# Kernel optimization log

Measured on AMD Instinct MI355X. Metric: run time of the kernel, lower is better.

## Reference

```python
import jax, jax.numpy as jnp
import numpy as np

B, S, H = 2, 1024, 2048
D = 256          # index_dimension = min(index.embedding_dimension, hidden_size)
R = 32           # LoRA rank
K = 4            # index_k neighbors per query token
N_DB = 100000    # rows in the external index


def setup_inputs() -> dict:
    key = jax.random.key(0)
    ks = jax.random.split(key, 7)
    return {
        "hidden_states": jax.random.normal(ks[0], (B, S, H), jnp.float32),
        "db_keys": jax.random.normal(ks[1], (N_DB, D), jnp.float32),
        "db_values": jax.random.normal(ks[2], (N_DB, D), jnp.float32),
        "wq_in": jax.random.normal(ks[3], (H, R), jnp.float32) * 0.02,
        "wq_out": jax.random.normal(ks[4], (R, D), jnp.float32) * 0.02,
        "wv_in": jax.random.normal(ks[5], (D, R), jnp.float32) * 0.02,
        "wv_out": jax.random.normal(ks[6], (R, H), jnp.float32) * 0.02,
    }


def reference(hidden_states, db_keys, db_values, wq_in, wq_out, wv_in, wv_out):
    b, s, h = hidden_states.shape
    d = wq_out.shape[1]
    # query LoRA projection: hidden -> r -> index_dim
    q = (hidden_states @ wq_in) @ wq_out            # [B, S, D]

    # external k-NN lookup (exact L2 top-k over index table), no_grad in torch
    qf = q.reshape(b * s, d)                        # [B*S, D]
    qn = jnp.sum(qf * qf, axis=-1, keepdims=True)   # [B*S, 1]
    kn = jnp.sum(db_keys * db_keys, axis=-1)        # [N_DB]
    dist = qn - 2.0 * (qf @ db_keys.T) + kn[None, :]  # [B*S, N_DB]
    _, idx = jax.lax.top_k(-dist, K)                # [B*S, K] nearest neighbors

    # gather KV and reshape to [B, S*K, D] (matches torch view calls)
    kv_key = jax.lax.stop_gradient(db_keys[idx]).reshape(b, s * K, d)
    kv_val = jax.lax.stop_gradient(db_values[idx]).reshape(b, s * K, d)

    # SDPA, is_causal=True with Lq != Lk: top-left aligned tril mask (j <= i)
    scale = 1.0 / np.sqrt(d).astype(np.float32)
    scores = jnp.einsum('bqd,bkd->bqk', q, kv_key) * scale  # [B, S, S*K]
    mask = jnp.arange(s * K)[None, :] <= jnp.arange(s)[:, None]
    scores = jnp.where(mask[None, :, :], scores, jnp.finfo(scores.dtype).min)
    attn = jax.nn.softmax(scores, axis=-1)
    out = jnp.einsum('bqk,bkd->bqd', attn, kv_val)  # [B, S, D]

    # value LoRA projection: index_dim -> r -> hidden
    return (out @ wv_in) @ wv_out                   # [B, S, H]
```

## Files before the change

### kernel.cpp

```cpp
#include <hip/hip_runtime.h>
#include <cfloat>

#define B_   2
#define S_   1024
#define H_   2048
#define D_   256
#define R_   32
#define K_   4
#define NDB_ 100000

#define TSEL 256
#define NSEL (B_ * TSEL)

#define NCHUNK     61
#define CHUNK_ROWS 1664
#define TILES      13
#define NT         128
#define MT         64
#define KC         64
#define LSTR       68

#define NEG_INF  (-3.0e38f)
#define IDX_MAX  0x7fffffff

#define OFF_Q     0
#define OFF_KN    0x200000
#define OFF_PS    0x280000
#define OFF_PI    0x300000
#define OFF_IDX   0x380000
#define OFF_CAND  0x3A0000
#define OFF_KVT   0x400000
#define OFF_AO    0x600000
#define OFF_KVV   0x800000
#define OFF_DBK16 0xA00000

typedef unsigned short ushort_t;
typedef unsigned int   uint_t;
typedef __attribute__((ext_vector_type(8)))  __bf16 bf16x8;
typedef __attribute__((ext_vector_type(16))) float  f32x16;

__device__ __forceinline__ void ins4(float sc, int n, float s[4], int id[4]) {
  if (sc > s[3] || (sc == s[3] && n < id[3])) {
    s[3] = sc; id[3] = n;
#pragma unroll
    for (int k = 3; k > 0; --k) {
      if (s[k] > s[k - 1] || (s[k] == s[k - 1] && id[k] < id[k - 1])) {
        float ts = s[k]; s[k] = s[k - 1]; s[k - 1] = ts;
        int ti = id[k]; id[k] = id[k - 1]; id[k - 1] = ti;
      }
    }
  }
}

__device__ __forceinline__ uint_t bfpack(float a, float b) {
  uint_t ua = __float_as_uint(a), ub = __float_as_uint(b);
  ua = (ua + 0x7fffu + ((ua >> 16) & 1u)) >> 16;
  ub = (ub + 0x7fffu + ((ub >> 16) & 1u)) >> 16;
  return ua | (ub << 16);
}

__global__ __launch_bounds__(256) void k_compute_q(
    const float* __restrict__ hidden, const float* __restrict__ wq_in,
    const float* __restrict__ wq_out, float* __restrict__ q) {
  __shared__ float hrow[H_];
  __shared__ float part[8][R_];
  __shared__ float q1[R_];
  const int m = blockIdx.x;
  const int t = threadIdx.x;
  const float* hp = hidden + (size_t)m * H_;
  ((float4*)hrow)[t]       = ((const float4*)hp)[t];
  ((float4*)hrow)[t + 256] = ((const float4*)hp)[t + 256];
  __syncthreads();
  const int r = t & 31, c = t >> 5;
  float p = 0.f;
#pragma unroll 4
  for (int e = c * 256; e < c * 256 + 256; ++e)
    p = fmaf(hrow[e], wq_in[(size_t)e * R_ + r], p);
  part[c][r] = p;
  __syncthreads();
  if (t < R_) {
    float s = 0.f;
#pragma unroll
    for (int cc = 0; cc < 8; ++cc) s += part[cc][t];
    q1[t] = s;
  }
  __syncthreads();
  float acc = 0.f;
#pragma unroll
  for (int rr = 0; rr < R_; ++rr) acc = fmaf(q1[rr], wq_out[rr * D_ + t], acc);
  q[(size_t)m * D_ + t] = acc;
}

__global__ __launch_bounds__(256) void k_kn_cvt(const float* __restrict__ dbk,
                                               float* __restrict__ kn,
                                               ushort_t* __restrict__ dbk16) {
  const int w = threadIdx.x >> 6, l = threadIdx.x & 63;
  const int n = blockIdx.x * 4 + w;
  if (n >= NDB_) return;
  const float4 v = ((const float4*)(dbk + (size_t)n * D_))[l];
  uint2 p; p.x = bfpack(v.x, v.y); p.y = bfpack(v.z, v.w);
  ((uint2*)(dbk16 + (size_t)n * D_))[l] = p;
  float s = v.x * v.x + v.y * v.y + v.z * v.z + v.w * v.w;
#pragma unroll
  for (int off = 32; off; off >>= 1) s += __shfl_down(s, off);
  if (l == 0) kn[n] = s;
}

__global__ __launch_bounds__(256) void k_kn(const float* __restrict__ dbk,
                                            float* __restrict__ kn) {
  const int w = threadIdx.x >> 6, l = threadIdx.x & 63;
  const int n = blockIdx.x * 4 + w;
  if (n >= NDB_) return;
  const float4 v = ((const float4*)(dbk + (size_t)n * D_))[l];
  float s = v.x * v.x + v.y * v.y + v.z * v.z + v.w * v.w;
#pragma unroll
  for (int off = 32; off; off >>= 1) s += __shfl_down(s, off);
  if (l == 0) kn[n] = s;
}

__global__ __launch_bounds__(256, 2) void k_knn_mfma(
    const float* __restrict__ q, const ushort_t* __restrict__ dbk16,
    const float* __restrict__ kn, float* __restrict__ pscore,
    int* __restrict__ pidx) {
  __shared__ __align__(16) char smem[65536];
  ushort_t* sA = (ushort_t*)smem;
  ushort_t* sB = (ushort_t*)(smem + 32768);
  float*    sS = (float*)(smem + 32768);

  const int tid = threadIdx.x;
  const int wv = tid >> 6, ln = tid & 63;
  const int lm = ln & 31, lh = ln >> 5;
  const int tx = tid & 15, ty = tid >> 4;
  const int qb = blockIdx.x, chunk = blockIdx.y;
  const int row_base = chunk * CHUNK_ROWS;

  {
    const int m = tid & 63, cg = tid >> 6;
    const int sq = qb * MT + m;
    const float* qp = q + ((size_t)((sq >> 8) * S_ + (sq & 255))) * D_;
#pragma unroll
    for (int cc = 0; cc < 8; ++cc) {
      const int c = cg * 8 + cc;
      const float4 v0 = *(const float4*)(qp + c * 8);
      const float4 v1 = *(const float4*)(qp + c * 8 + 4);
      uint4 pk;
      pk.x = bfpack(v0.x, v0.y); pk.y = bfpack(v0.z, v0.w);
      pk.z = bfpack(v1.x, v1.y); pk.w = bfpack(v1.z, v1.w);
      *(uint4*)&sA[(m * 32 + (c ^ (m & 7))) * 8] = pk;
    }
  }

  float s4[4][4]; int i4[4][4];
#pragma unroll
  for (int a = 0; a < 4; ++a)
#pragma unroll
    for (int b = 0; b < 4; ++b) { s4[a][b] = NEG_INF; i4[a][b] = IDX_MAX; }

  for (int tile = 0; tile < TILES; ++tile) {
    const int row0 = row_base + tile * NT;
    if (row0 >= NDB_) break;

    f32x16 acc0, acc1;
#pragma unroll
    for (int r = 0; r < 16; ++r) { acc0[r] = 0.f; acc1[r] = 0.f; }

    for (int kh = 0; kh < 2; ++kh) {
      __syncthreads();
      {
        const int n_in = ln >> 4;
        const int p    = ln & 15;
#pragma unroll
        for (int i = 0; i < 8; ++i) {
          const int nloc = wv * 32 + i * 4 + n_in;
          int krow = row0 + nloc; if (krow >= NDB_) krow = NDB_ - 1;
          const int c = p ^ (nloc & 7);
          const ushort_t* gp = dbk16 + (size_t)krow * D_ + (kh * 16 + c) * 8;
          ushort_t* lp = sB + (size_t)(wv * 32 + i * 4) * 128;
          __builtin_amdgcn_global_load_lds(
              (const __attribute__((address_space(1))) void*)gp,
              (__attribute__((address_space(3))) void*)lp, 16, 0, 0);
        }
      }
      __syncthreads();
      const int nB = wv * 32 + lm;
      const int bswz = nB & 7;
#pragma unroll
      for (int ks = 0; ks < 8; ++ks) {
        const int cA = kh * 16 + ks * 2 + lh;
        const bf16x8 a0 = *(const bf16x8*)&sA[(lm * 32 + (cA ^ (lm & 7))) * 8];
        const bf16x8 a1 = *(const bf16x8*)&sA[((32 + lm) * 32 + (cA ^ (lm & 7))) * 8];
        const bf16x8 bb = *(const bf16x8*)&sB[(nB * 16 + ((ks * 2 + lh) ^ bswz)) * 8];
        acc0 = __builtin_amdgcn_mfma_f32_32x32x16_bf16(a0, bb, acc0, 0, 0, 0);
        acc1 = __builtin_amdgcn_mfma_f32_32x32x16_bf16(a1, bb, acc1, 0, 0, 0);
      }
    }
    __syncthreads();

    {
      const int n = (tid >> 6) * 32 + lm;
#pragma unroll
      for (int r = 0; r < 16; ++r) {
        const int mrow = (r & 3) + 8 * (r >> 2) + 4 * lh;
        sS[mrow * 128 + n]        = acc0[r];
        sS[(32 + mrow) * 128 + n] = acc1[r];
      }
    }
    __syncthreads();

    {
      const int nbase = row0 + tx * 8;
      float knv[8]; int nok[8];
#pragma unroll
      for (int j = 0; j < 8; ++j) {
        nok[j] = (nbase + j < NDB_);
        knv[j] = nok[j] ? kn[nbase + j] : 0.f;
      }
#pragma unroll
      for (int qi = 0; qi < 4; ++qi) {
        const int m = ty * 4 + qi;
        const float4 v0 = *(const float4*)&sS[m * 128 + tx * 8];
        const float4 v1 = *(const float4*)&sS[m * 128 + tx * 8 + 4];
        const float sv[8] = {v0.x, v0.y, v0.z, v0.w, v1.x, v1.y, v1.z, v1.w};
        float v[8];
#pragma unroll
        for (int j = 0; j < 8; ++j)
          v[j] = nok[j] ? fmaf(2.f, sv[j], -knv[j]) : NEG_INF;
        const float mx = fmaxf(fmaxf(fmaxf(v[0], v[1]), fmaxf(v[2], v[3])),
                               fmaxf(fmaxf(v[4], v[5]), fmaxf(v[6], v[7])));
        if (mx >= s4[qi][3]) {
#pragma unroll
          for (int j = 0; j < 8; ++j)
            if (nok[j]) ins4(v[j], nbase + j, s4[qi], i4[qi]);
        }
      }
    }
  }

  __syncthreads();
  float* cs = (float*)smem;
  int*   ci = (int*)(smem + 64 * 65 * 4);
#pragma unroll
  for (int qi = 0; qi < 4; ++qi)
#pragma unroll
    for (int k = 0; k < 4; ++k) {
      cs[(ty * 4 + qi) * 65 + tx * 4 + k] = s4[qi][k];
      ci[(ty * 4 + qi) * 65 + tx * 4 + k] = i4[qi][k];
    }
  __syncthreads();
  if (tid < 64) {
    float fs[4]; int fi[4];
#pragma unroll
    for (int k = 0; k < 4; ++k) { fs[k] = NEG_INF; fi[k] = IDX_MAX; }
    for (int c = 0; c < 64; ++c)
      ins4(cs[tid * 65 + c], ci[tid * 65 + c], fs, fi);
    const int sq = qb * MT + tid;
    float* po = pscore + ((size_t)sq * NCHUNK + chunk) * 4;
    int*   io = pidx   + ((size_t)sq * NCHUNK + chunk) * 4;
#pragma unroll
    for (int k = 0; k < 4; ++k) { po[k] = fs[k]; io[k] = fi[k]; }
  }
}

__global__ __launch_bounds__(256) void k_knn_partial(
    const float* __restrict__ q, const float* __restrict__ dbk,
    const float* __restrict__ kn, float* __restrict__ pscore,
    int* __restrict__ pidx) {
  __shared__ float smem[3 * KC * LSTR];
  float* sA  = smem;
  float* sB0 = smem + KC * LSTR;
  float* sB1 = smem + 2 * KC * LSTR;
  const int tid = threadIdx.x;
  const int tx = tid & 15, ty = tid >> 4;
  const int chunk = blockIdx.x, qb = blockIdx.y;
  const int arq = tid >> 2;
  const int aqd = (tid & 3) * 4;
  const int brk = tid >> 1;
  const int bh  = tid & 1;
  const int bcol = ((brk >> 3) << 2) | (brk & 3);
  float* sBw = (brk & 4) ? sB1 : sB0;
  const int sq_a = qb * MT + arq;
  const float* qsrc = q + ((size_t)((sq_a >> 8) * S_ + (sq_a & 255))) * D_;
  float s4[4][4]; int i4[4][4];
#pragma unroll
  for (int a = 0; a < 4; ++a)
#pragma unroll
    for (int b = 0; b < 4; ++b) { s4[a][b] = NEG_INF; i4[a][b] = IDX_MAX; }
  const int row_base = chunk * CHUNK_ROWS;
  for (int tile = 0; tile < TILES; ++tile) {
    const int row0 = row_base + tile * NT;
    if (row0 >= NDB_) break;
    int krow = row0 + brk; if (krow >= NDB_) krow = NDB_ - 1;
    const float* ksrc = dbk + (size_t)krow * D_;
    float acc[4][8];
#pragma unroll
    for (int a = 0; a < 4; ++a)
#pragma unroll
      for (int b = 0; b < 8; ++b) acc[a][b] = 0.f;
    for (int kc = 0; kc < 4; ++kc) {
      __syncthreads();
#pragma unroll
      for (int p = 0; p < 4; ++p) {
        const int kkl = p * 16 + aqd;
        const float4 v = *(const float4*)(qsrc + kc * KC + kkl);
        sA[(kkl + 0) * LSTR + arq] = v.x;
        sA[(kkl + 1) * LSTR + arq] = v.y;
        sA[(kkl + 2) * LSTR + arq] = v.z;
        sA[(kkl + 3) * LSTR + arq] = v.w;
      }
#pragma unroll
      for (int p = 0; p < 8; ++p) {
        const int kkl = bh * 32 + p * 4;
        const float4 v = *(const float4*)(ksrc + kc * KC + kkl);
        sBw[(kkl + 0) * LSTR + bcol] = v.x;
        sBw[(kkl + 1) * LSTR + bcol] = v.y;
        sBw[(kkl + 2) * LSTR + bcol] = v.z;
        sBw[(kkl + 3) * LSTR + bcol] = v.w;
      }
      __syncthreads();
#pragma unroll 4
      for (int kk = 0; kk < KC; ++kk) {
        const float4 a  = *(const float4*)&sA [kk * LSTR + ty * 4];
        const float4 b0 = *(const float4*)&sB0[kk * LSTR + tx * 4];
        const float4 b1 = *(const float4*)&sB1[kk * LSTR + tx * 4];
        const float av[4] = {a.x, a.y, a.z, a.w};
        const float bv[8] = {b0.x, b0.y, b0.z, b0.w, b1.x, b1.y, b1.z, b1.w};
#pragma unroll
        for (int qi = 0; qi < 4; ++qi)
#pragma unroll
          for (int nj = 0; nj < 8; ++nj)
            acc[qi][nj] = fmaf(av[qi], bv[nj], acc[qi][nj]);
      }
    }
#pragma unroll
    for (int nj = 0; nj < 8; ++nj) {
      const int n = row0 + tx * 8 + nj;
      if (n < NDB_) {
        const float knj = kn[n];
        ins4(2.f * acc[0][nj] - knj, n, s4[0], i4[0]);
        ins4(2.f * acc[1][nj] - knj, n, s4[1], i4[1]);
        ins4(2.f * acc[2][nj] - knj, n, s4[2], i4[2]);
        ins4(2.f * acc[3][nj] - knj, n, s4[3], i4[3]);
      }
    }
  }
  __syncthreads();
  float* cs = smem;
  int*   ci = (int*)(smem + 64 * 65);
#pragma unroll
  for (int qi = 0; qi < 4; ++qi)
#pragma unroll
    for (int k = 0; k < 4; ++k) {
      cs[(ty * 4 + qi) * 65 + tx * 4 + k] = s4[qi][k];
      ci[(ty * 4 + qi) * 65 + tx * 4 + k] = i4[qi][k];
    }
  __syncthreads();
  if (tid < 64) {
    float fs[4]; int fi[4];
#pragma unroll
    for (int k = 0; k < 4; ++k) { fs[k] = NEG_INF; fi[k] = IDX_MAX; }
    for (int c = 0; c < 64; ++c)
      ins4(cs[tid * 65 + c], ci[tid * 65 + c], fs, fi);
    const int sq = qb * MT + tid;
    float* po = pscore + ((size_t)sq * NCHUNK + chunk) * 4;
    int*   io = pidx   + ((size_t)sq * NCHUNK + chunk) * 4;
#pragma unroll
    for (int k = 0; k < 4; ++k) { po[k] = fs[k]; io[k] = fi[k]; }
  }
}

template <int RANKS>
__device__ __forceinline__ void merge_top(const float* __restrict__ pscore,
                                          const int* __restrict__ pidx,
                                          int* __restrict__ outp) {
  const int sq = blockIdx.x, l = threadIdx.x;
  float s4[4]; int i4[4];
#pragma unroll
  for (int k = 0; k < 4; ++k) { s4[k] = NEG_INF; i4[k] = IDX_MAX; }
  for (int c = l; c < NCHUNK * 4; c += 64)
    ins4(pscore[(size_t)sq * NCHUNK * 4 + c], pidx[(size_t)sq * NCHUNK * 4 + c], s4, i4);
#pragma unroll
  for (int r = 0; r < RANKS; ++r) {
    float s = s4[0]; int i = i4[0];
#pragma unroll
    for (int off = 32; off; off >>= 1) {
      float so = __shfl_down(s, off); int io = __shfl_down(i, off);
      if (so > s || (so == s && io < i)) { s = so; i = io; }
    }
    const float sw = __shfl(s, 0); const int iw = __shfl(i, 0);
    if (l == 0) outp[sq * RANKS + r] = iw;
    if (s4[0] == sw && i4[0] == iw) {
      s4[0] = s4[1]; i4[0] = i4[1];
      s4[1] = s4[2]; i4[1] = i4[2];
      s4[2] = s4[3]; i4[2] = i4[3];
      s4[3] = NEG_INF; i4[3] = IDX_MAX;
    }
  }
}

__global__ __launch_bounds__(64) void k_knn_merge4(const float* __restrict__ ps,
                                                   const int* __restrict__ pi,
                                                   int* __restrict__ knn_idx) {
  merge_top<4>(ps, pi, knn_idx);
}
__global__ __launch_bounds__(64) void k_knn_merge16(const float* __restrict__ ps,
                                                    const int* __restrict__ pi,
                                                    int* __restrict__ cand) {
  merge_top<16>(ps, pi, cand);
}

__global__ __launch_bounds__(256) void k_rescore(const float* __restrict__ q,
                                                 const float* __restrict__ dbk,
                                                 const float* __restrict__ kn,
                                                 const int* __restrict__ cand,
                                                 int* __restrict__ knn_idx) {
  __shared__ float scs[16];
  __shared__ int   sci[16];
  const int sq = blockIdx.x, wv = threadIdx.x >> 6, l = threadIdx.x & 63;
  const float* qp = q + ((size_t)((sq >> 8) * S_ + (sq & 255))) * D_;
  const float4 qv = ((const float4*)qp)[l];
  for (int cc = wv; cc < 16; cc += 4) {
    const int n = cand[sq * 16 + cc];
    const float4 kv = ((const float4*)(dbk + (size_t)n * D_))[l];
    float s = qv.x * kv.x + qv.y * kv.y + qv.z * kv.z + qv.w * kv.w;
#pragma unroll
    for (int off = 32; off; off >>= 1) s += __shfl_down(s, off);
    if (l == 0) { scs[cc] = 2.f * s - kn[n]; sci[cc] = n; }
  }
  __syncthreads();
  if (threadIdx.x == 0) {
    float s4[4]; int i4[4];
#pragma unroll
    for (int k = 0; k < 4; ++k) { s4[k] = NEG_INF; i4[k] = IDX_MAX; }
#pragma unroll
    for (int c = 0; c < 16; ++c) ins4(scs[c], sci[c], s4, i4);
#pragma unroll
    for (int k = 0; k < 4; ++k) knn_idx[sq * 4 + k] = i4[k];
  }
}

__global__ __launch_bounds__(256) void k_gather(const float* __restrict__ dbk,
                                                const float* __restrict__ dbv,
                                                const int* __restrict__ knn_idx,
                                                float* __restrict__ kvT,
                                                float* __restrict__ kvV) {
  const int b = blockIdx.x >> 6, j0 = (blockIdx.x & 63) * 16;
  const int w = threadIdx.x >> 6, l = threadIdx.x & 63;
  float* dstT = kvT + (size_t)b * D_ * 1024;
  float* dstV = kvV + (size_t)b * 1024 * D_;
  for (int jj = w; jj < 16; jj += 4) {
    const int j = j0 + jj;
    const int row = knn_idx[b * 1024 + j];
    const float4 kv = ((const float4*)(dbk + (size_t)row * D_))[l];
    dstT[(4 * l + 0) * 1024 + j] = kv.x;
    dstT[(4 * l + 1) * 1024 + j] = kv.y;
    dstT[(4 * l + 2) * 1024 + j] = kv.z;
    dstT[(4 * l + 3) * 1024 + j] = kv.w;
    const float4 vv = ((const float4*)(dbv + (size_t)row * D_))[l];
    ((float4*)(dstV + (size_t)j * D_))[l] = vv;
  }
}

__global__ __launch_bounds__(256) void k_attn(const float* __restrict__ qarr,
                                              const float* __restrict__ kvT,
                                              const float* __restrict__ kvV,
                                              float* __restrict__ attout) {
  __shared__ float qrow[D_];
  __shared__ float attw[1024];
  __shared__ float red1[4], red2[4];
  const int b = blockIdx.x >> 10, i = blockIdx.x & 1023;
  const int t = threadIdx.x;
  const int nk = i + 1;
  qrow[t] = qarr[((size_t)b * S_ + i) * D_ + t];
  __syncthreads();
  const int cmax = (nk + 255) >> 8;
  const float scale = 0.0625f;
  float sc[4]; float mloc = NEG_INF;
#pragma unroll
  for (int c = 0; c < 4; ++c) {
    sc[c] = NEG_INF;
    if (c < cmax) {
      const int j = c * 256 + t;
      float a = 0.f;
      const float* kp = kvT + (size_t)b * D_ * 1024 + j;
#pragma unroll 8
      for (int d = 0; d < D_; ++d) a = fmaf(qrow[d], kp[(size_t)d * 1024], a);
      if (j < nk) sc[c] = a * scale;
    }
    mloc = fmaxf(mloc, sc[c]);
  }
#pragma unroll
  for (int off = 32; off; off >>= 1) mloc = fmaxf(mloc, __shfl_down(mloc, off));
  if ((t & 63) == 0) red1[t >> 6] = mloc;
  __syncthreads();
  const float mmax = fmaxf(fmaxf(red1[0], red1[1]), fmaxf(red1[2], red1[3]));
  float sloc = 0.f; float pv[4];
#pragma unroll
  for (int c = 0; c < 4; ++c) {
    pv[c] = (sc[c] > NEG_INF * 0.5f) ? __expf(sc[c] - mmax) : 0.f;
    sloc += pv[c];
  }
#pragma unroll
  for (int off = 32; off; off >>= 1) sloc += __shfl_down(sloc, off);
  if ((t & 63) == 0) red2[t >> 6] = sloc;
  __syncthreads();
  const float inv = 1.f / (red2[0] + red2[1] + red2[2] + red2[3]);
#pragma unroll
  for (int c = 0; c < 4; ++c)
    if (c < cmax) attw[c * 256 + t] = pv[c] * inv;
  __syncthreads();
  const float* vb = kvV + (size_t)b * 1024 * D_;
  float a0 = 0.f, a1 = 0.f, a2 = 0.f, a3 = 0.f;
  int j = 0;
  for (; j + 4 <= nk; j += 4) {
    a0 = fmaf(attw[j + 0], vb[(size_t)(j + 0) * D_ + t], a0);
    a1 = fmaf(attw[j + 1], vb[(size_t)(j + 1) * D_ + t], a1);
    a2 = fmaf(attw[j + 2], vb[(size_t)(j + 2) * D_ + t], a2);
    a3 = fmaf(attw[j + 3], vb[(size_t)(j + 3) * D_ + t], a3);
  }
  for (; j < nk; ++j) a0 = fmaf(attw[j], vb[(size_t)j * D_ + t], a0);
  attout[((size_t)b * S_ + i) * D_ + t] = (a0 + a1) + (a2 + a3);
}

__global__ __launch_bounds__(256) void k_out(const float* __restrict__ attout,
                                             const float* __restrict__ wv_in,
                                             const float* __restrict__ wv_out,
                                             float* __restrict__ y) {
  __shared__ float row[D_];
  __shared__ float part[8][R_];
  __shared__ float t32[R_];
  const int m = blockIdx.x, t = threadIdx.x;
  row[t] = attout[(size_t)m * D_ + t];
  __syncthreads();
  const int r = t & 31, c = t >> 5;
  float p = 0.f;
#pragma unroll
  for (int d = c * 32; d < c * 32 + 32; ++d)
    p = fmaf(row[d], wv_in[d * R_ + r], p);
  part[c][r] = p;
  __syncthreads();
  if (t < R_) {
    float s = 0.f;
#pragma unroll
    for (int cc = 0; cc < 8; ++cc) s += part[cc][t];
    t32[t] = s;
  }
  __syncthreads();
  for (int hh = t; hh < H_; hh += 256) {
    float a = 0.f;
#pragma unroll
    for (int rr = 0; rr < R_; ++rr) a = fmaf(t32[rr], wv_out[rr * H_ + hh], a);
    y[(size_t)m * H_ + hh] = a;
  }
}

extern "C" void kernel_launch(void* const* d_in, const int* in_sizes, int n_in,
                              void* d_out, int out_size, void* d_ws, size_t ws_size,
                              hipStream_t stream) {
  const float* hidden  = (const float*)d_in[0];
  const float* db_keys = (const float*)d_in[1];
  const float* db_vals = (const float*)d_in[2];
  const float* wq_in   = (const float*)d_in[3];
  const float* wq_out  = (const float*)d_in[4];
  const float* wv_in   = (const float*)d_in[5];
  const float* wv_out  = (const float*)d_in[6];
  float* out = (float*)d_out;

  char* ws = (char*)d_ws;
  float*    q      = (float*)(ws + OFF_Q);
  float*    kn     = (float*)(ws + OFF_KN);
  float*    ps     = (float*)(ws + OFF_PS);
  int*      pi     = (int*)  (ws + OFF_PI);
  int*      idx    = (int*)  (ws + OFF_IDX);
  int*      cand   = (int*)  (ws + OFF_CAND);
  float*    kvT    = (float*)(ws + OFF_KVT);
  float*    attout = (float*)(ws + OFF_AO);
  float*    kvV    = (float*)(ws + OFF_KVV);
  ushort_t* dbk16  = (ushort_t*)(ws + OFF_DBK16);

  const size_t need = (size_t)OFF_DBK16 + (size_t)NDB_ * D_ * 2;

  k_compute_q<<<B_ * S_, 256, 0, stream>>>(hidden, wq_in, wq_out, q);
  if (ws_size >= need) {
    k_kn_cvt<<<(NDB_ + 3) / 4, 256, 0, stream>>>(db_keys, kn, dbk16);
    k_knn_mfma<<<dim3(8, NCHUNK), 256, 0, stream>>>(q, dbk16, kn, ps, pi);
    k_knn_merge16<<<NSEL, 64, 0, stream>>>(ps, pi, cand);
    k_rescore<<<NSEL, 256, 0, stream>>>(q, db_keys, kn, cand, idx);
  } else {
    k_kn<<<(NDB_ + 3) / 4, 256, 0, stream>>>(db_keys, kn);
    k_knn_partial<<<dim3(NCHUNK, 8), 256, 0, stream>>>(q, db_keys, kn, ps, pi);
    k_knn_merge4<<<NSEL, 64, 0, stream>>>(ps, pi, idx);
  }
  k_gather<<<2 * 64, 256, 0, stream>>>(db_keys, db_vals, idx, kvT, kvV);
  k_attn<<<B_ * S_, 256, 0, stream>>>(q, kvT, kvV, attout);
  k_out<<<B_ * S_, 256, 0, stream>>>(attout, wv_in, wv_out, out);
}
```

Measured before the change: 544.4 us.

## Restructure kNN MFMA kernel to hold DB keys in registers and score in-register

The MFMA kNN kernel now loads each wave's 32 database rows directly from global memory into registers as the A operand and keeps 128 query rows in LDS as the B operand. This removes the per-tile LDS staging of DB keys, the score round-trip through shared memory and most barriers, and top-4 selection now runs directly on the accumulator registers. The kn buffer is padded with large sentinel values so out-of-range rows drop out without bounds checks. The chunk count and tile sizes change (131 chunks of 768 rows), and partial-result buffers are aliased onto the later KV workspace. The trade-off is much higher register pressure (16 bf16x8 fragments plus four accumulators) and more partial results to merge.

```diff
diff --git a/kernel.cpp b/kernel.cpp
--- a/kernel.cpp
+++ b/kernel.cpp
@@ -8,14 +8,19 @@
 #define R_   32
 #define K_   4
 #define NDB_ 100000
+#define KN_PAD 2048
 
 #define TSEL 256
 #define NSEL (B_ * TSEL)
 
-#define NCHUNK     61
-#define CHUNK_ROWS 1664
-#define TILES      13
-#define NT         128
+#define NCHUNK     131
+#define CHUNK_ROWS 768
+#define TILES      6
+#define MTQ        128
+
+#define FB_NCHUNK     61
+#define FB_CHUNK_ROWS 1664
+#define FB_TILES      13
 #define MT         64
 #define KC         64
 #define LSTR       68
@@ -25,14 +30,12 @@
 
 #define OFF_Q     0
 #define OFF_KN    0x200000
-#define OFF_PS    0x280000
-#define OFF_PI    0x300000
-#define OFF_IDX   0x380000
-#define OFF_CAND  0x3A0000
-#define OFF_KVT   0x400000
-#define OFF_AO    0x600000
-#define OFF_KVV   0x800000
-#define OFF_DBK16 0xA00000
+#define OFF_IDX   0x280000
+#define OFF_CAND  0x290000
+#define OFF_KVT   0x300000
+#define OFF_AO    0x500000
+#define OFF_KVV   0x700000
+#define OFF_DBK16 0x900000
 
 typedef unsigned short ushort_t;
 typedef unsigned int   uint_t;
@@ -96,7 +99,8 @@
                                                ushort_t* __restrict__ dbk16) {
   const int w = threadIdx.x >> 6, l = threadIdx.x & 63;
   const int n = blockIdx.x * 4 + w;
-  if (n >= NDB_) return;
+  if (n >= NDB_ + KN_PAD) return;
+  if (n >= NDB_) { if (l == 0) kn[n] = 1.0e30f; return; }
   const float4 v = ((const float4*)(dbk + (size_t)n * D_))[l];
   uint2 p; p.x = bfpack(v.x, v.y); p.y = bfpack(v.z, v.w);
   ((uint2*)(dbk16 + (size_t)n * D_))[l] = p;
@@ -122,138 +126,112 @@
     const float* __restrict__ q, const ushort_t* __restrict__ dbk16,
     const float* __restrict__ kn, float* __restrict__ pscore,
     int* __restrict__ pidx) {
-  __shared__ __align__(16) char smem[65536];
-  ushort_t* sA = (ushort_t*)smem;
-  ushort_t* sB = (ushort_t*)(smem + 32768);
-  float*    sS = (float*)(smem + 32768);
+  __shared__ __align__(16) ushort_t sA16[MTQ * 256];
 
   const int tid = threadIdx.x;
-  const int wv = tid >> 6, ln = tid & 63;
+  const int w = tid >> 6, ln = tid & 63;
   const int lm = ln & 31, lh = ln >> 5;
-  const int tx = tid & 15, ty = tid >> 4;
   const int qb = blockIdx.x, chunk = blockIdx.y;
   const int row_base = chunk * CHUNK_ROWS;
 
   {
-    const int m = tid & 63, cg = tid >> 6;
-    const int sq = qb * MT + m;
+    const int m = tid >> 1, h = tid & 1;
+    const int sq = qb * MTQ + m;
     const float* qp = q + ((size_t)((sq >> 8) * S_ + (sq & 255))) * D_;
 #pragma unroll
-    for (int cc = 0; cc < 8; ++cc) {
-      const int c = cg * 8 + cc;
+    for (int ci = 0; ci < 16; ++ci) {
+      const int c = h * 16 + ci;
       const float4 v0 = *(const float4*)(qp + c * 8);
       const float4 v1 = *(const float4*)(qp + c * 8 + 4);
       uint4 pk;
       pk.x = bfpack(v0.x, v0.y); pk.y = bfpack(v0.z, v0.w);
       pk.z = bfpack(v1.x, v1.y); pk.w = bfpack(v1.z, v1.w);
-      *(uint4*)&sA[(m * 32 + (c ^ (m & 7))) * 8] = pk;
-    }
-  }
+      *(uint4*)&sA16[(m * 32 + (c ^ (m & 7))) * 8] = pk;
+    }
+  }
+  __syncthreads();
 
   float s4[4][4]; int i4[4][4];
 #pragma unroll
-  for (int a = 0; a < 4; ++a)
-#pragma unroll
-    for (int b = 0; b < 4; ++b) { s4[a][b] = NEG_INF; i4[a][b] = IDX_MAX; }
+  for (int g = 0; g < 4; ++g)
+#pragma unroll
+    for (int k = 0; k < 4; ++k) { s4[g][k] = NEG_INF; i4[g][k] = IDX_MAX; }
+
+  const int aswz = lm & 7;
 
   for (int tile = 0; tile < TILES; ++tile) {
-    const int row0 = row_base + tile * NT;
-    if (row0 >= NDB_) break;
-
-    f32x16 acc0, acc1;
-#pragma unroll
-    for (int r = 0; r < 16; ++r) { acc0[r] = 0.f; acc1[r] = 0.f; }
-
-    for (int kh = 0; kh < 2; ++kh) {
-      __syncthreads();
-      {
-        const int n_in = ln >> 4;
-        const int p    = ln & 15;
-#pragma unroll
-        for (int i = 0; i < 8; ++i) {
-          const int nloc = wv * 32 + i * 4 + n_in;
-          int krow = row0 + nloc; if (krow >= NDB_) krow = NDB_ - 1;
-          const int c = p ^ (nloc & 7);
-          const ushort_t* gp = dbk16 + (size_t)krow * D_ + (kh * 16 + c) * 8;
-          ushort_t* lp = sB + (size_t)(wv * 32 + i * 4) * 128;
-          __builtin_amdgcn_global_load_lds(
-              (const __attribute__((address_space(1))) void*)gp,
-              (__attribute__((address_space(3))) void*)lp, 16, 0, 0);
+    const int row0 = row_base + tile * 128;
+    int rowA = row0 + w * 32 + lm; if (rowA >= NDB_) rowA = NDB_ - 1;
+    const ushort_t* ap = dbk16 + (size_t)rowA * D_ + lh * 8;
+
+    bf16x8 aF[16];
+#pragma unroll
+    for (int ks = 0; ks < 16; ++ks)
+      aF[ks] = *(const bf16x8*)(ap + ks * 16);
+
+    const int knb = row0 + w * 32 + lh * 4;
+    const float4 kf0 = *(const float4*)&kn[knb];
+    const float4 kf1 = *(const float4*)&kn[knb + 8];
+    const float4 kf2 = *(const float4*)&kn[knb + 16];
+    const float4 kf3 = *(const float4*)&kn[knb + 24];
+    const float karr[16] = {kf0.x, kf0.y, kf0.z, kf0.w, kf1.x, kf1.y, kf1.z, kf1.w,
+                            kf2.x, kf2.y, kf2.z, kf2.w, kf3.x, kf3.y, kf3.z, kf3.w};
+
+    f32x16 acc[4];
+#pragma unroll
+    for (int g = 0; g < 4; ++g)
+#pragma unroll
+      for (int r = 0; r < 16; ++r) acc[g][r] = 0.f;
+
+#pragma unroll
+    for (int ks = 0; ks < 16; ++ks) {
+      const int pos = ((ks * 2 + lh) ^ aswz) * 8;
+#pragma unroll
+      for (int g = 0; g < 4; ++g) {
+        const bf16x8 bq = *(const bf16x8*)&sA16[(g * 32 + lm) * 256 + pos];
+        acc[g] = __builtin_amdgcn_mfma_f32_32x32x16_bf16(aF[ks], bq, acc[g], 0, 0, 0);
+      }
+    }
+
+#pragma unroll
+    for (int g = 0; g < 4; ++g) {
+      float v[16];
+#pragma unroll
+      for (int r = 0; r < 16; ++r) v[r] = fmaf(2.f, acc[g][r], -karr[r]);
+      float mx = v[0];
+#pragma unroll
+      for (int r = 1; r < 16; ++r) mx = fmaxf(mx, v[r]);
+      if (mx >= s4[g][3]) {
+#pragma unroll
+        for (int r = 0; r < 16; ++r) {
+          const int n = row0 + w * 32 + (r >> 2) * 8 + 4 * lh + (r & 3);
+          ins4(v[r], n, s4[g], i4[g]);
         }
       }
-      __syncthreads();
-      const int nB = wv * 32 + lm;
-      const int bswz = nB & 7;
-#pragma unroll
-      for (int ks = 0; ks < 8; ++ks) {
-        const int cA = kh * 16 + ks * 2 + lh;
-        const bf16x8 a0 = *(const bf16x8*)&sA[(lm * 32 + (cA ^ (lm & 7))) * 8];
-        const bf16x8 a1 = *(const bf16x8*)&sA[((32 + lm) * 32 + (cA ^ (lm & 7))) * 8];
-        const bf16x8 bb = *(const bf16x8*)&sB[(nB * 16 + ((ks * 2 + lh) ^ bswz)) * 8];
-        acc0 = __builtin_amdgcn_mfma_f32_32x32x16_bf16(a0, bb, acc0, 0, 0, 0);
-        acc1 = __builtin_amdgcn_mfma_f32_32x32x16_bf16(a1, bb, acc1, 0, 0, 0);
-      }
-    }
-    __syncthreads();
-
-    {
-      const int n = (tid >> 6) * 32 + lm;
-#pragma unroll
-      for (int r = 0; r < 16; ++r) {
-        const int mrow = (r & 3) + 8 * (r >> 2) + 4 * lh;
-        sS[mrow * 128 + n]        = acc0[r];
-        sS[(32 + mrow) * 128 + n] = acc1[r];
-      }
-    }
-    __syncthreads();
-
-    {
-      const int nbase = row0 + tx * 8;
-      float knv[8]; int nok[8];
-#pragma unroll
-      for (int j = 0; j < 8; ++j) {
-        nok[j] = (nbase + j < NDB_);
-        knv[j] = nok[j] ? kn[nbase + j] : 0.f;
-      }
-#pragma unroll
-      for (int qi = 0; qi < 4; ++qi) {
-        const int m = ty * 4 + qi;
-        const float4 v0 = *(const float4*)&sS[m * 128 + tx * 8];
-        const float4 v1 = *(const float4*)&sS[m * 128 + tx * 8 + 4];
-        const float sv[8] = {v0.x, v0.y, v0.z, v0.w, v1.x, v1.y, v1.z, v1.w};
-        float v[8];
-#pragma unroll
-        for (int j = 0; j < 8; ++j)
-          v[j] = nok[j] ? fmaf(2.f, sv[j], -knv[j]) : NEG_INF;
-        const float mx = fmaxf(fmaxf(fmaxf(v[0], v[1]), fmaxf(v[2], v[3])),
-                               fmaxf(fmaxf(v[4], v[5]), fmaxf(v[6], v[7])));
-        if (mx >= s4[qi][3]) {
-#pragma unroll
-          for (int j = 0; j < 8; ++j)
-            if (nok[j]) ins4(v[j], nbase + j, s4[qi], i4[qi]);
-        }
-      }
-    }
-  }
-
-  __syncthreads();
-  float* cs = (float*)smem;
-  int*   ci = (int*)(smem + 64 * 65 * 4);
-#pragma unroll
-  for (int qi = 0; qi < 4; ++qi)
+    }
+  }
+
+  __syncthreads();
+  float* cs = (float*)sA16;
+  int*   ci = (int*)((char*)sA16 + 128 * 33 * 4 + 64);
+#pragma unroll
+  for (int g = 0; g < 4; ++g) {
+    const int qrow = g * 32 + lm;
+    const int src = w * 8 + lh * 4;
 #pragma unroll
     for (int k = 0; k < 4; ++k) {
-      cs[(ty * 4 + qi) * 65 + tx * 4 + k] = s4[qi][k];
-      ci[(ty * 4 + qi) * 65 + tx * 4 + k] = i4[qi][k];
-    }
-  __syncthreads();
-  if (tid < 64) {
+      cs[qrow * 33 + src + k] = s4[g][k];
+      ci[qrow * 33 + src + k] = i4[g][k];
+    }
+  }
+  __syncthreads();
+  if (tid < MTQ) {
     float fs[4]; int fi[4];
 #pragma unroll
     for (int k = 0; k < 4; ++k) { fs[k] = NEG_INF; fi[k] = IDX_MAX; }
-    for (int c = 0; c < 64; ++c)
-      ins4(cs[tid * 65 + c], ci[tid * 65 + c], fs, fi);
-    const int sq = qb * MT + tid;
+    for (int c = 0; c < 32; ++c)
+      ins4(cs[tid * 33 + c], ci[tid * 33 + c], fs, fi);
+    const int sq = qb * MTQ + tid;
     float* po = pscore + ((size_t)sq * NCHUNK + chunk) * 4;
     int*   io = pidx   + ((size_t)sq * NCHUNK + chunk) * 4;
 #pragma unroll
@@ -285,9 +263,9 @@
   for (int a = 0; a < 4; ++a)
 #pragma unroll
     for (int b = 0; b < 4; ++b) { s4[a][b] = NEG_INF; i4[a][b] = IDX_MAX; }
-  const int row_base = chunk * CHUNK_ROWS;
-  for (int tile = 0; tile < TILES; ++tile) {
-    const int row0 = row_base + tile * NT;
+  const int row_base = chunk * FB_CHUNK_ROWS;
+  for (int tile = 0; tile < FB_TILES; ++tile) {
+    const int row0 = row_base + tile * 128;
     if (row0 >= NDB_) break;
     int krow = row0 + brk; if (krow >= NDB_) krow = NDB_ - 1;
     const float* ksrc = dbk + (size_t)krow * D_;
@@ -361,8 +339,8 @@
     for (int c = 0; c < 64; ++c)
       ins4(cs[tid * 65 + c], ci[tid * 65 + c], fs, fi);
     const int sq = qb * MT + tid;
-    float* po = pscore + ((size_t)sq * NCHUNK + chunk) * 4;
-    int*   io = pidx   + ((size_t)sq * NCHUNK + chunk) * 4;
+    float* po = pscore + ((size_t)sq * FB_NCHUNK + chunk) * 4;
+    int*   io = pidx   + ((size_t)sq * FB_NCHUNK + chunk) * 4;
 #pragma unroll
     for (int k = 0; k < 4; ++k) { po[k] = fs[k]; io[k] = fi[k]; }
   }
@@ -371,13 +349,13 @@
 template <int RANKS>
 __device__ __forceinline__ void merge_top(const float* __restrict__ pscore,
                                           const int* __restrict__ pidx,
-                                          int* __restrict__ outp) {
+                                          int* __restrict__ outp, int nch) {
   const int sq = blockIdx.x, l = threadIdx.x;
   float s4[4]; int i4[4];
 #pragma unroll
   for (int k = 0; k < 4; ++k) { s4[k] = NEG_INF; i4[k] = IDX_MAX; }
-  for (int c = l; c < NCHUNK * 4; c += 64)
-    ins4(pscore[(size_t)sq * NCHUNK * 4 + c], pidx[(size_t)sq * NCHUNK * 4 + c], s4, i4);
+  for (int c = l; c < nch * 4; c += 64)
+    ins4(pscore[(size_t)sq * nch * 4 + c], pidx[(size_t)sq * nch * 4 + c], s4, i4);
 #pragma unroll
   for (int r = 0; r < RANKS; ++r) {
     float s = s4[0]; int i = i4[0];
@@ -399,13 +377,13 @@
 
 __global__ __launch_bounds__(64) void k_knn_merge4(const float* __restrict__ ps,
                                                    const int* __restrict__ pi,
-                                                   int* __restrict__ knn_idx) {
-  merge_top<4>(ps, pi, knn_idx);
+                                                   int* __restrict__ knn_idx, int nch) {
+  merge_top<4>(ps, pi, knn_idx, nch);
 }
 __global__ __launch_bounds__(64) void k_knn_merge16(const float* __restrict__ ps,
                                                     const int* __restrict__ pi,
-                                                    int* __restrict__ cand) {
-  merge_top<16>(ps, pi, cand);
+                                                    int* __restrict__ cand, int nch) {
+  merge_top<16>(ps, pi, cand, nch);
 }
 
 __global__ __launch_bounds__(256) void k_rescore(const float* __restrict__ q,
@@ -568,27 +546,27 @@
   char* ws = (char*)d_ws;
   float*    q      = (float*)(ws + OFF_Q);
   float*    kn     = (float*)(ws + OFF_KN);
-  float*    ps     = (float*)(ws + OFF_PS);
-  int*      pi     = (int*)  (ws + OFF_PI);
   int*      idx    = (int*)  (ws + OFF_IDX);
   int*      cand   = (int*)  (ws + OFF_CAND);
   float*    kvT    = (float*)(ws + OFF_KVT);
   float*    attout = (float*)(ws + OFF_AO);
   float*    kvV    = (float*)(ws + OFF_KVV);
   ushort_t* dbk16  = (ushort_t*)(ws + OFF_DBK16);
+  float*    ps     = (float*)(ws + OFF_KVT);
+  int*      pi     = (int*)  (ws + OFF_KVV);
 
   const size_t need = (size_t)OFF_DBK16 + (size_t)NDB_ * D_ * 2;
 
   k_compute_q<<<B_ * S_, 256, 0, stream>>>(hidden, wq_in, wq_out, q);
   if (ws_size >= need) {
-    k_kn_cvt<<<(NDB_ + 3) / 4, 256, 0, stream>>>(db_keys, kn, dbk16);
-    k_knn_mfma<<<dim3(8, NCHUNK), 256, 0, stream>>>(q, dbk16, kn, ps, pi);
-    k_knn_merge16<<<NSEL, 64, 0, stream>>>(ps, pi, cand);
+    k_kn_cvt<<<(NDB_ + KN_PAD + 3) / 4, 256, 0, stream>>>(db_keys, kn, dbk16);
+    k_knn_mfma<<<dim3(NSEL / MTQ, NCHUNK), 256, 0, stream>>>(q, dbk16, kn, ps, pi);
+    k_knn_merge16<<<NSEL, 64, 0, stream>>>(ps, pi, cand, NCHUNK);
     k_rescore<<<NSEL, 256, 0, stream>>>(q, db_keys, kn, cand, idx);
   } else {
     k_kn<<<(NDB_ + 3) / 4, 256, 0, stream>>>(db_keys, kn);
-    k_knn_partial<<<dim3(NCHUNK, 8), 256, 0, stream>>>(q, db_keys, kn, ps, pi);
-    k_knn_merge4<<<NSEL, 64, 0, stream>>>(ps, pi, idx);
+    k_knn_partial<<<dim3(FB_NCHUNK, 8), 256, 0, stream>>>(q, db_keys, kn, ps, pi);
+    k_knn_merge4<<<NSEL, 64, 0, stream>>>(ps, pi, idx, FB_NCHUNK);
   }
   k_gather<<<2 * 64, 256, 0, stream>>>(db_keys, db_vals, idx, kvT, kvV);
   k_attn<<<B_ * S_, 256, 0, stream>>>(q, kvT, kvV, attout);
```

After: 646.2 us. 18.7% more time.
